# Performance work log

Hardware: AMD Instinct MI355X
Metric: run time of the kernel (lower is better)

The kernel has to match this reference:

```python
import jax, jax.numpy as jnp
import numpy as np

N_QUBITS = 8
N_LAYERS = 2


def _apply_1q(state, U, wire):
    # state: (B, 2, ..., 2) with N_QUBITS qubit axes; U: (2,2) complex, shared over batch
    s = jnp.moveaxis(state, 1 + wire, 1)
    shp = s.shape
    out = jnp.einsum('ij,bjr->bir', U, s.reshape(shp[0], 2, -1)).reshape(shp)
    return jnp.moveaxis(out, 1, 1 + wire)


def _apply_cnot(state, c, t):
    s = jnp.moveaxis(state, (1 + c, 1 + t), (1, 2))  # (B, ctrl, tgt, ...)
    s_new = jnp.stack([s[:, 0], jnp.flip(s[:, 1], axis=1)], axis=1)
    return jnp.moveaxis(s_new, (1, 2), (1 + c, 1 + t))


def _circuit(angles, q_weights):
    # angles: (B, N) real; q_weights: (L, N, 3) real
    B = angles.shape[0]
    N = N_QUBITS
    # AngleEmbedding with RY on |0...0> -> product state [cos(a/2), sin(a/2)] per qubit
    half = angles * 0.5
    state = jnp.ones((B, 1), dtype=jnp.complex64)
    for i in range(N):
        v = jnp.stack([jnp.cos(half[:, i]), jnp.sin(half[:, i])], axis=-1).astype(jnp.complex64)
        state = (state[:, :, None] * v[:, None, :]).reshape(B, -1)
    state = state.reshape((B,) + (2,) * N)
    # StronglyEntanglingLayers: per layer, Rot(phi,theta,omega) on each wire then CNOT ring
    L = q_weights.shape[0]
    for l in range(L):
        for i in range(N):
            phi = q_weights[l, i, 0]
            theta = q_weights[l, i, 1]
            omega = q_weights[l, i, 2]
            c = jnp.cos(theta * 0.5).astype(jnp.complex64)
            s_ = jnp.sin(theta * 0.5).astype(jnp.complex64)
            ep = jnp.exp(-0.5j * (phi + omega).astype(jnp.complex64))
            em = jnp.exp(-0.5j * (phi - omega).astype(jnp.complex64))
            # Rot = RZ(omega) RY(theta) RZ(phi)
            U = jnp.stack([jnp.stack([ep * c, -jnp.conj(em) * s_]),
                           jnp.stack([em * s_, jnp.conj(ep) * c])])
            state = _apply_1q(state, U, i)
        r = l % (N - 1) + 1  # default range pattern of StronglyEntanglingLayers
        for i in range(N):
            state = _apply_cnot(state, i, (i + r) % N)
    # <Z_i> = P(bit_i=0) - P(bit_i=1)
    probs = jnp.real(state * jnp.conj(state))
    zs = []
    for i in range(N):
        pm = jnp.moveaxis(probs, 1 + i, 1).reshape(B, 2, -1).sum(-1)
        zs.append(pm[:, 0] - pm[:, 1])
    return jnp.stack(zs, axis=-1)  # (B, N) real


def setup_inputs() -> dict:
    key = jax.random.key(0)
    k1, k2, k3, k4 = jax.random.split(key, 4)
    B = 32768
    pca_x = jax.random.normal(k1, (B, N_QUBITS), dtype=jnp.float32)
    q_weights = jax.random.uniform(k2, (N_LAYERS, N_QUBITS, 3), dtype=jnp.float32) * (2.0 * np.pi)
    W = jax.random.normal(k3, (N_QUBITS, 64), dtype=jnp.float32) * 0.35
    b = jax.random.normal(k4, (64,), dtype=jnp.float32) * 0.02
    gamma = jnp.ones((64,), dtype=jnp.float32)
    beta = jnp.zeros((64,), dtype=jnp.float32)
    return {"pca_x": pca_x, "q_weights": q_weights, "W": W, "b": b, "gamma": gamma, "beta": beta}


def reference(pca_x, q_weights, W, b, gamma, beta):
    angles = jax.nn.sigmoid(pca_x) * jnp.pi  # (B, 8)
    z = _circuit(angles, q_weights).astype(pca_x.dtype)  # (B, 8) PauliZ expvals
    h = z @ W + b  # (B, 64)
    mu = jnp.mean(h, axis=-1, keepdims=True)
    var = jnp.mean((h - mu) ** 2, axis=-1, keepdims=True)
    hn = (h - mu) / jnp.sqrt(var + 1e-5) * gamma + beta
    return jax.nn.gelu(hn, approximate=False)
```

## Files before the change

kernel.cpp:

```cpp
#include <hip/hip_runtime.h>
#include <math.h>

#define DEVFN __device__ __forceinline__

typedef __attribute__((ext_vector_type(8))) _Float16 f16x8;
typedef __attribute__((ext_vector_type(4))) float f32x4;

DEVFN float shxor(float v, int m) { return __shfl_xor(v, m, 64); }

template<int W>
DEVFN void rot_gate(int lane, float (&sr)[4], float (&si)[4], const float* u) {
  const float u00r=u[0], u00i=u[1], u01r=u[2], u01i=u[3];
  const float u10r=u[4], u10i=u[5], u11r=u[6], u11i=u[7];
  if constexpr (W <= 5) {
    constexpr int M = 1 << (5 - W);
    const bool hi = (lane & M) != 0;
    const float cmr = hi ? u11r : u00r, cmi = hi ? u11i : u00i;
    const float cor = hi ? u10r : u01r, coi = hi ? u10i : u01i;
    #pragma unroll
    for (int k = 0; k < 4; ++k) {
      float orr = shxor(sr[k], M);
      float oii = shxor(si[k], M);
      float nr = cmr*sr[k] - cmi*si[k] + cor*orr - coi*oii;
      float ni = cmr*si[k] + cmi*sr[k] + cor*oii + coi*orr;
      sr[k] = nr; si[k] = ni;
    }
  } else {
    constexpr int KB = (W == 6) ? 2 : 1;
    #pragma unroll
    for (int k0 = 0; k0 < 4; ++k0) {
      if ((k0 & KB) == 0) {
        const int k1 = k0 | KB;
        float ar = sr[k0], ai = si[k0];
        float br = sr[k1], bi = si[k1];
        sr[k0] = u00r*ar - u00i*ai + u01r*br - u01i*bi;
        si[k0] = u00r*ai + u00i*ar + u01r*bi + u01i*br;
        sr[k1] = u10r*ar - u10i*ai + u11r*br - u11i*bi;
        si[k1] = u10r*ai + u10i*ar + u11r*bi + u11i*br;
      }
    }
  }
}

template<int C, int T>
DEVFN void cnot_gate(int lane, float (&sr)[4], float (&si)[4]) {
  constexpr int PC = 7 - C, PT = 7 - T;
  if constexpr (PT >= 2) {
    constexpr int M = 1 << (PT - 2);
    #pragma unroll
    for (int k = 0; k < 4; ++k) {
      float orr = shxor(sr[k], M);
      float oii = shxor(si[k], M);
      bool ctrl;
      if constexpr (PC >= 2) ctrl = ((lane >> (PC - 2)) & 1) != 0;
      else                   ctrl = ((k >> PC) & 1) != 0;
      if (ctrl) { sr[k] = orr; si[k] = oii; }
    }
  } else {
    float tr[4], ti[4];
    #pragma unroll
    for (int k = 0; k < 4; ++k) { tr[k] = sr[k]; ti[k] = si[k]; }
    #pragma unroll
    for (int k = 0; k < 4; ++k) {
      bool ctrl;
      if constexpr (PC >= 2) ctrl = ((lane >> (PC - 2)) & 1) != 0;
      else                   ctrl = ((k >> PC) & 1) != 0;
      if (ctrl) { sr[k] = tr[k ^ (1 << PT)]; si[k] = ti[k ^ (1 << PT)]; }
    }
  }
}

__global__ __launch_bounds__(64) void qsb_prep(
    const float* __restrict__ qw, const float* __restrict__ Wm,
    const float* __restrict__ bias,
    _Float16* __restrict__ Bfrag, float* __restrict__ stats) {
  __shared__ float uL[16 * 8];
  int bid = blockIdx.x;
  int lane = threadIdx.x;
  if (bid < 256) {
    if (lane < 16) {
      int l = lane >> 3, i = lane & 7;
      float phi = qw[l*24 + i*3 + 0];
      float th  = qw[l*24 + i*3 + 1];
      float om  = qw[l*24 + i*3 + 2];
      float cth = cosf(0.5f*th), sth = sinf(0.5f*th);
      float ap = 0.5f*(phi+om), am = 0.5f*(phi-om);
      float cap = cosf(ap), sap = sinf(ap);
      float cam = cosf(am), sam = sinf(am);
      float* u = &uL[lane*8];
      u[0] =  cap*cth; u[1] = -sap*cth;
      u[2] = -cam*sth; u[3] = -sam*sth;
      u[4] =  cam*sth; u[5] = -sam*sth;
      u[6] =  cap*cth; u[7] =  sap*cth;
    }
    __syncthreads();
    int col = bid;
    float sr[4], si[4];
    #pragma unroll
    for (int k = 0; k < 4; ++k) { sr[k] = (lane*4 + k == col) ? 1.f : 0.f; si[k] = 0.f; }
    rot_gate<0>(lane, sr, si, &uL[0*8]);
    rot_gate<1>(lane, sr, si, &uL[1*8]);
    rot_gate<2>(lane, sr, si, &uL[2*8]);
    rot_gate<3>(lane, sr, si, &uL[3*8]);
    rot_gate<4>(lane, sr, si, &uL[4*8]);
    rot_gate<5>(lane, sr, si, &uL[5*8]);
    rot_gate<6>(lane, sr, si, &uL[6*8]);
    rot_gate<7>(lane, sr, si, &uL[7*8]);
    cnot_gate<0,1>(lane, sr, si);
    cnot_gate<1,2>(lane, sr, si);
    cnot_gate<2,3>(lane, sr, si);
    cnot_gate<3,4>(lane, sr, si);
    cnot_gate<4,5>(lane, sr, si);
    cnot_gate<5,6>(lane, sr, si);
    cnot_gate<6,7>(lane, sr, si);
    cnot_gate<7,0>(lane, sr, si);
    rot_gate<0>(lane, sr, si, &uL[(8+0)*8]);
    rot_gate<1>(lane, sr, si, &uL[(8+1)*8]);
    rot_gate<2>(lane, sr, si, &uL[(8+2)*8]);
    rot_gate<3>(lane, sr, si, &uL[(8+3)*8]);
    rot_gate<4>(lane, sr, si, &uL[(8+4)*8]);
    rot_gate<5>(lane, sr, si, &uL[(8+5)*8]);
    rot_gate<6>(lane, sr, si, &uL[(8+6)*8]);
    rot_gate<7>(lane, sr, si, &uL[(8+7)*8]);
    cnot_gate<0,2>(lane, sr, si);
    cnot_gate<1,3>(lane, sr, si);
    cnot_gate<2,4>(lane, sr, si);
    cnot_gate<3,5>(lane, sr, si);
    cnot_gate<4,6>(lane, sr, si);
    cnot_gate<5,7>(lane, sr, si);
    cnot_gate<6,0>(lane, sr, si);
    cnot_gate<7,1>(lane, sr, si);
    const int ks = col >> 5, kg = (col >> 3) & 3, e = col & 7;
    #pragma unroll
    for (int k = 0; k < 4; ++k) {
      int a = lane*4 + k;
      int ch = a >> 5, nf = (a >> 4) & 1, cf = a & 15;
      int pos = (kg*16 + cf)*8 + e;
      Bfrag[((ch*4 + nf    )*8 + ks)*512 + pos] = (_Float16)sr[k];
      Bfrag[((ch*4 + 2 + nf)*8 + ks)*512 + pos] = (_Float16)si[k];
    }
  } else {
    int t = lane;
    {
      int i = t >> 3, j = t & 7;
      float s = 0.f;
      for (int c = 0; c < 64; ++c) s += Wm[i*64 + c] * Wm[j*64 + c];
      stats[16 + t] = s * 0.015625f;
    }
    if (t < 8) {
      float s = 0.f, sb = 0.f;
      for (int c = 0; c < 64; ++c) { float w = Wm[t*64 + c]; s += w; sb += w * bias[c]; }
      stats[t]     = s * 0.015625f;
      stats[8 + t] = 2.f * sb * 0.015625f;
    }
    if (t == 0) {
      float s = 0.f, s2 = 0.f;
      for (int c = 0; c < 64; ++c) { s += bias[c]; s2 += bias[c]*bias[c]; }
      stats[80] = s * 0.015625f;
      stats[81] = s2 * 0.015625f;
    }
  }
}

__global__ __launch_bounds__(256, 4) void qsb_main(
    const float* __restrict__ pca, const _Float16* __restrict__ Bfrag,
    const float* __restrict__ statsG,
    const float* __restrict__ Wm, const float* __restrict__ bias,
    const float* __restrict__ gamma, const float* __restrict__ beta,
    float* __restrict__ out, int B) {
  __shared__ __align__(16) _Float16 A3[8192];
  __shared__ __align__(16) _Float16 YL[4 * 1280];
  __shared__ float zpart[2304];
  __shared__ float zrow[256];
  __shared__ float musig[64];
  __shared__ float Wl[512];
  __shared__ float biasL[64], gammaL[64], betaL[64];
  __shared__ float statsL[82];

  const int tid = threadIdx.x;
  const int wid = tid >> 6, lane = tid & 63;
  const int cfrag = lane & 15, kgrp = lane >> 4;
  const int r0 = blockIdx.x * 32;

  #pragma unroll
  for (int i = tid; i < 512; i += 256) Wl[i] = Wm[i];
  if (tid >= 256 - 64) {
    int t = tid - (256 - 64);
    biasL[t] = bias[t]; gammaL[t] = gamma[t]; betaL[t] = beta[t];
  }
  if (tid < 82) statsL[tid] = statsG[tid];

  f16x8 sfrag;
  #pragma unroll
  for (int e = 0; e < 8; ++e) {
    float v;
    if      (cfrag == 0) v = 1.f;
    else if (cfrag == 1) v = (kgrp & 2) ? -1.f : 1.f;
    else if (cfrag == 2) v = (kgrp & 1) ? -1.f : 1.f;
    else if (cfrag == 3) v = (e & 4)    ? -1.f : 1.f;
    else if (cfrag == 4) v = (e & 2)    ? -1.f : 1.f;
    else if (cfrag == 5) v = (e & 1)    ? -1.f : 1.f;
    else v = 0.f;
    sfrag[e] = (_Float16)v;
  }

  {
    const int rl = tid >> 3, tq = tid & 7;
    const int r = r0 + rl;
    float cv[8], sv[8];
    #pragma unroll
    for (int w = 0; w < 8; ++w) { cv[w] = 1.f; sv[w] = 0.f; }
    if (r < B) {
      #pragma unroll
      for (int w = 0; w < 8; ++w) {
        float x = pca[r*8 + w];
        float sg = __builtin_amdgcn_rcpf(1.f + __expf(-x));
        float ang = 1.5707963267948966f * sg;
        cv[w] = __cosf(ang); sv[w] = __sinf(ang);
      }
    }
    float base = ((tq & 4) ? sv[0] : cv[0]) * ((tq & 2) ? sv[1] : cv[1])
               * ((tq & 1) ? sv[2] : cv[2]);
    float arr[32];
    arr[0] = base;
    #pragma unroll
    for (int p = 0; p < 5; ++p) {
      const int w = 7 - p;
      const int sz = 1 << p;
      #pragma unroll
      for (int i = 0; i < (1 << p); ++i) {
        arr[i + sz] = arr[i] * sv[w];
        arr[i]      = arr[i] * cv[w];
      }
    }
    _Float16* dstBase = &A3[((tq*2 + (rl >> 4))*16 + (rl & 15))*32];
    #pragma unroll
    for (int ib = 0; ib < 4; ++ib) {
      f16x8 v;
      #pragma unroll
      for (int j = 0; j < 8; ++j) v[j] = (_Float16)arr[ib*8 + j];
      *(f16x8*)(dstBase + (ib ^ (tq & 3))*8) = v;
    }
  }
  __syncthreads();

  _Float16* Yw = &YL[wid * 1280];
  const _Float16* BwBase = Bfrag + (size_t)(wid*2) * 16384 + lane*8;

  f32x4 acc[2][4];
  #pragma unroll
  for (int m = 0; m < 2; ++m)
    #pragma unroll
    for (int q = 0; q < 4; ++q) acc[m][q] = (f32x4){0.f, 0.f, 0.f, 0.f};

  f16x8 bk[3][4];
  #pragma unroll
  for (int q = 0; q < 4; ++q) bk[0][q] = *(const f16x8*)(BwBase + 0*512 + q*4096);
  #pragma unroll
  for (int q = 0; q < 4; ++q) bk[1][q] = *(const f16x8*)(BwBase + 1*512 + q*4096);

  #pragma unroll
  for (int s = 0; s < 16; ++s) {
    const int ks = s & 7;
    const int bi = s % 3;
    if (s + 2 < 16) {
      const int bj = (s + 2) % 3;
      const int c2 = (s + 2) >> 3, ks2 = (s + 2) & 7;
      const _Float16* p2 = BwBase + c2*16384 + ks2*512;
      #pragma unroll
      for (int q = 0; q < 4; ++q) bk[bj][q] = *(const f16x8*)(p2 + q*4096);
    }
    {
      f16x8 af0 = *(const f16x8*)&A3[((ks*2 + 0)*16 + cfrag)*32 + (kgrp ^ (ks & 3))*8];
      f16x8 af1 = *(const f16x8*)&A3[((ks*2 + 1)*16 + cfrag)*32 + (kgrp ^ (ks & 3))*8];
      #pragma unroll
      for (int q = 0; q < 4; ++q) {
        acc[0][q] = __builtin_amdgcn_mfma_f32_16x16x32_f16(af0, bk[bi][q], acc[0][q], 0, 0, 0);
        acc[1][q] = __builtin_amdgcn_mfma_f32_16x16x32_f16(af1, bk[bi][q], acc[1][q], 0, 0, 0);
      }
    }
    if (ks == 7) {
      const int ch = wid*2 + (s >> 3);
      #pragma unroll
      for (int m = 0; m < 2; ++m) {
        #pragma unroll
        for (int nf = 0; nf < 2; ++nf) {
          #pragma unroll
          for (int j = 0; j < 4; ++j) {
            float re = acc[m][nf][j], im = acc[m][2 + nf][j];
            float p = re*re + im*im;
            Yw[m*640 + (kgrp*4 + j)*40 + nf*16 + cfrag] = (_Float16)p;
          }
        }
      }
      #pragma unroll
      for (int m = 0; m < 2; ++m) {
        f16x8 yfrag = *(const f16x8*)&Yw[m*640 + (lane & 15)*40 + kgrp*8];
        f32x4 d = __builtin_amdgcn_mfma_f32_16x16x32_f16(yfrag, sfrag, (f32x4){0.f,0.f,0.f,0.f}, 0, 0, 0);
        if (cfrag < 6) {
          #pragma unroll
          for (int j = 0; j < 4; ++j)
            zpart[(ch*32 + m*16 + kgrp*4 + j)*9 + cfrag] = d[j];
        }
      }
      #pragma unroll
      for (int m = 0; m < 2; ++m)
        #pragma unroll
        for (int q = 0; q < 4; ++q) acc[m][q] = (f32x4){0.f, 0.f, 0.f, 0.f};
    }
  }
  __syncthreads();

  {
    const int row = tid >> 3, w = tid & 7;
    const int slot = (w < 3) ? 0 : (w - 2);
    const int sm = (w == 0) ? 4 : (w == 1) ? 2 : (w == 2) ? 1 : 0;
    float z = 0.f;
    #pragma unroll
    for (int ch = 0; ch < 8; ++ch) {
      float v = zpart[(ch*32 + row)*9 + slot];
      z += (ch & sm) ? -v : v;
    }
    zrow[row*8 + w] = z;
    f32x4 zlo = *(const f32x4*)&zrow[row*8];
    f32x4 zhi = *(const f32x4*)&zrow[row*8 + 4];
    float zj[8] = {zlo[0], zlo[1], zlo[2], zlo[3], zhi[0], zhi[1], zhi[2], zhi[3]};
    float qi = statsL[8 + w];
    #pragma unroll
    for (int j = 0; j < 8; ++j) qi += statsL[16 + w*8 + j] * zj[j];
    float e2p = zj[w] * qi;
    float mup = statsL[w] * zj[w];
    e2p += shxor(e2p, 1); e2p += shxor(e2p, 2); e2p += shxor(e2p, 4);
    mup += shxor(mup, 1); mup += shxor(mup, 2); mup += shxor(mup, 4);
    if (w == 0) {
      float mu = mup + statsL[80];
      float e2 = e2p + statsL[81];
      float var = e2 - mu*mu;
      musig[row*2]     = mu;
      musig[row*2 + 1] = rsqrtf(fmaxf(var, 0.f) + 1e-5f);
    }
  }

  #pragma unroll
  for (int rr = 0; rr < 8; ++rr) {
    const int row = wid*8 + rr;
    const int gr = r0 + row;
    float h = biasL[lane];
    #pragma unroll
    for (int i = 0; i < 8; ++i) h = fmaf(zrow[row*8 + i], Wl[i*64 + lane], h);
    float hn = (h - musig[row*2]) * musig[row*2 + 1] * gammaL[lane] + betaL[lane];
    float ge = 0.5f * hn * (1.f + erff(hn * 0.70710678118654752f));
    if (gr < B) out[gr*64 + lane] = ge;
  }
}

extern "C" void kernel_launch(void* const* d_in, const int* in_sizes, int n_in,
                              void* d_out, int out_size, void* d_ws, size_t ws_size,
                              hipStream_t stream) {
  const float* pca   = (const float*)d_in[0];
  const float* qw    = (const float*)d_in[1];
  const float* Wm    = (const float*)d_in[2];
  const float* bias  = (const float*)d_in[3];
  const float* gamma = (const float*)d_in[4];
  const float* beta  = (const float*)d_in[5];
  float* out = (float*)d_out;

  _Float16* Bfrag = (_Float16*)d_ws;
  float* stats = (float*)((char*)d_ws + 512*256*2);

  int B = in_sizes[0] / 8;

  hipLaunchKernelGGL(qsb_prep, dim3(257), dim3(64), 0, stream, qw, Wm, bias, Bfrag, stats);
  int blocks = (B + 31) / 32;
  hipLaunchKernelGGL(qsb_main, dim3(blocks), dim3(256), 0, stream,
                     pca, Bfrag, stats, Wm, bias, gamma, beta, out, B);
}
```

Baseline: 28.58 us.

## Double rows per block so each B fragment feeds four MFMA row tiles

Result: slower. 29.27 us (+2.4%).

```diff
diff --git a/kernel.cpp b/kernel.cpp
--- a/kernel.cpp
+++ b/kernel.cpp
@@ -162,17 +162,17 @@
   }
 }
 
-__global__ __launch_bounds__(256, 4) void qsb_main(
+__global__ __launch_bounds__(256, 2) void qsb_main(
     const float* __restrict__ pca, const _Float16* __restrict__ Bfrag,
     const float* __restrict__ statsG,
     const float* __restrict__ Wm, const float* __restrict__ bias,
     const float* __restrict__ gamma, const float* __restrict__ beta,
     float* __restrict__ out, int B) {
-  __shared__ __align__(16) _Float16 A3[8192];
-  __shared__ __align__(16) _Float16 YL[4 * 1280];
-  __shared__ float zpart[2304];
-  __shared__ float zrow[256];
-  __shared__ float musig[64];
+  __shared__ __align__(16) _Float16 A3[16384];
+  __shared__ __align__(16) _Float16 YL[4 * 2560];
+  __shared__ float zpart[4608];
+  __shared__ float zrow[512];
+  __shared__ float musig[128];
   __shared__ float Wl[512];
   __shared__ float biasL[64], gammaL[64], betaL[64];
   __shared__ float statsL[82];
@@ -180,7 +180,7 @@
   const int tid = threadIdx.x;
   const int wid = tid >> 6, lane = tid & 63;
   const int cfrag = lane & 15, kgrp = lane >> 4;
-  const int r0 = blockIdx.x * 32;
+  const int r0 = blockIdx.x * 64;
 
   #pragma unroll
   for (int i = tid; i < 512; i += 256) Wl[i] = Wm[i];
@@ -205,7 +205,7 @@
   }
 
   {
-    const int rl = tid >> 3, tq = tid & 7;
+    const int rl = tid >> 2, tq = tid & 3;
     const int r = r0 + rl;
     float cv[8], sv[8];
     #pragma unroll
@@ -219,12 +219,11 @@
         cv[w] = __cosf(ang); sv[w] = __sinf(ang);
       }
     }
-    float base = ((tq & 4) ? sv[0] : cv[0]) * ((tq & 2) ? sv[1] : cv[1])
-               * ((tq & 1) ? sv[2] : cv[2]);
-    float arr[32];
+    float base = ((tq & 2) ? sv[0] : cv[0]) * ((tq & 1) ? sv[1] : cv[1]);
+    float arr[64];
     arr[0] = base;
     #pragma unroll
-    for (int p = 0; p < 5; ++p) {
+    for (int p = 0; p < 6; ++p) {
       const int w = 7 - p;
       const int sz = 1 << p;
       #pragma unroll
@@ -233,23 +232,27 @@
         arr[i]      = arr[i] * cv[w];
       }
     }
-    _Float16* dstBase = &A3[((tq*2 + (rl >> 4))*16 + (rl & 15))*32];
-    #pragma unroll
-    for (int ib = 0; ib < 4; ++ib) {
+    const int m = rl >> 4, cf = rl & 15;
+    const int cfx = (cf >> 1) & 3;
+    #pragma unroll
+    for (int ib = 0; ib < 8; ++ib) {
+      const int ks = tq*2 + (ib >> 2);
+      const int slot = (ib & 3) ^ (ks & 3) ^ cfx;
       f16x8 v;
       #pragma unroll
       for (int j = 0; j < 8; ++j) v[j] = (_Float16)arr[ib*8 + j];
-      *(f16x8*)(dstBase + (ib ^ (tq & 3))*8) = v;
+      *(f16x8*)&A3[((ks*4 + m)*16 + cf)*32 + slot*8] = v;
     }
   }
   __syncthreads();
 
-  _Float16* Yw = &YL[wid * 1280];
+  _Float16* Yw = &YL[wid * 2560];
   const _Float16* BwBase = Bfrag + (size_t)(wid*2) * 16384 + lane*8;
-
-  f32x4 acc[2][4];
-  #pragma unroll
-  for (int m = 0; m < 2; ++m)
+  const int cfx = (cfrag >> 1) & 3;
+
+  f32x4 acc[4][4];
+  #pragma unroll
+  for (int m = 0; m < 4; ++m)
     #pragma unroll
     for (int q = 0; q < 4; ++q) acc[m][q] = (f32x4){0.f, 0.f, 0.f, 0.f};
 
@@ -271,18 +274,22 @@
       for (int q = 0; q < 4; ++q) bk[bj][q] = *(const f16x8*)(p2 + q*4096);
     }
     {
-      f16x8 af0 = *(const f16x8*)&A3[((ks*2 + 0)*16 + cfrag)*32 + (kgrp ^ (ks & 3))*8];
-      f16x8 af1 = *(const f16x8*)&A3[((ks*2 + 1)*16 + cfrag)*32 + (kgrp ^ (ks & 3))*8];
+      const int slot = (kgrp ^ (ks & 3) ^ cfx)*8;
+      f16x8 af[4];
+      #pragma unroll
+      for (int m = 0; m < 4; ++m)
+        af[m] = *(const f16x8*)&A3[((ks*4 + m)*16 + cfrag)*32 + slot];
       #pragma unroll
       for (int q = 0; q < 4; ++q) {
-        acc[0][q] = __builtin_amdgcn_mfma_f32_16x16x32_f16(af0, bk[bi][q], acc[0][q], 0, 0, 0);
-        acc[1][q] = __builtin_amdgcn_mfma_f32_16x16x32_f16(af1, bk[bi][q], acc[1][q], 0, 0, 0);
+        #pragma unroll
+        for (int m = 0; m < 4; ++m)
+          acc[m][q] = __builtin_amdgcn_mfma_f32_16x16x32_f16(af[m], bk[bi][q], acc[m][q], 0, 0, 0);
       }
     }
     if (ks == 7) {
       const int ch = wid*2 + (s >> 3);
       #pragma unroll
-      for (int m = 0; m < 2; ++m) {
+      for (int m = 0; m < 4; ++m) {
         #pragma unroll
         for (int nf = 0; nf < 2; ++nf) {
           #pragma unroll
@@ -294,31 +301,32 @@
         }
       }
       #pragma unroll
-      for (int m = 0; m < 2; ++m) {
+      for (int m = 0; m < 4; ++m) {
         f16x8 yfrag = *(const f16x8*)&Yw[m*640 + (lane & 15)*40 + kgrp*8];
         f32x4 d = __builtin_amdgcn_mfma_f32_16x16x32_f16(yfrag, sfrag, (f32x4){0.f,0.f,0.f,0.f}, 0, 0, 0);
         if (cfrag < 6) {
           #pragma unroll
           for (int j = 0; j < 4; ++j)
-            zpart[(ch*32 + m*16 + kgrp*4 + j)*9 + cfrag] = d[j];
+            zpart[(ch*64 + m*16 + kgrp*4 + j)*9 + cfrag] = d[j];
         }
       }
       #pragma unroll
-      for (int m = 0; m < 2; ++m)
+      for (int m = 0; m < 4; ++m)
         #pragma unroll
         for (int q = 0; q < 4; ++q) acc[m][q] = (f32x4){0.f, 0.f, 0.f, 0.f};
     }
   }
   __syncthreads();
 
-  {
-    const int row = tid >> 3, w = tid & 7;
+  #pragma unroll
+  for (int h = 0; h < 2; ++h) {
+    const int row = h*32 + (tid >> 3), w = tid & 7;
     const int slot = (w < 3) ? 0 : (w - 2);
     const int sm = (w == 0) ? 4 : (w == 1) ? 2 : (w == 2) ? 1 : 0;
     float z = 0.f;
     #pragma unroll
     for (int ch = 0; ch < 8; ++ch) {
-      float v = zpart[(ch*32 + row)*9 + slot];
+      float v = zpart[(ch*64 + row)*9 + slot];
       z += (ch & sm) ? -v : v;
     }
     zrow[row*8 + w] = z;
@@ -342,15 +350,18 @@
   }
 
   #pragma unroll
-  for (int rr = 0; rr < 8; ++rr) {
-    const int row = wid*8 + rr;
-    const int gr = r0 + row;
-    float h = biasL[lane];
-    #pragma unroll
-    for (int i = 0; i < 8; ++i) h = fmaf(zrow[row*8 + i], Wl[i*64 + lane], h);
-    float hn = (h - musig[row*2]) * musig[row*2 + 1] * gammaL[lane] + betaL[lane];
-    float ge = 0.5f * hn * (1.f + erff(hn * 0.70710678118654752f));
-    if (gr < B) out[gr*64 + lane] = ge;
+  for (int h = 0; h < 2; ++h) {
+    #pragma unroll
+    for (int rr = 0; rr < 8; ++rr) {
+      const int row = h*32 + wid*8 + rr;
+      const int gr = r0 + row;
+      float hv = biasL[lane];
+      #pragma unroll
+      for (int i = 0; i < 8; ++i) hv = fmaf(zrow[row*8 + i], Wl[i*64 + lane], hv);
+      float hn = (hv - musig[row*2]) * musig[row*2 + 1] * gammaL[lane] + betaL[lane];
+      float ge = 0.5f * hn * (1.f + erff(hn * 0.70710678118654752f));
+      if (gr < B) out[gr*64 + lane] = ge;
+    }
   }
 }
 
@@ -371,7 +382,7 @@
   int B = in_sizes[0] / 8;
 
   hipLaunchKernelGGL(qsb_prep, dim3(257), dim3(64), 0, stream, qw, Wm, bias, Bfrag, stats);
-  int blocks = (B + 31) / 32;
+  int blocks = (B + 63) / 64;
   hipLaunchKernelGGL(qsb_main, dim3(blocks), dim3(256), 0, stream,
                      pca, Bfrag, stats, Wm, bias, gamma, beta, out, B);
 }
```

## Give each wave 16 whole rows across all chunks, building A fragments in registers

Applied to the files above, without the earlier changes.

New measurement: 50.60 us. +77.0%, slower.

```diff
diff --git a/kernel.cpp b/kernel.cpp
--- a/kernel.cpp
+++ b/kernel.cpp
@@ -168,11 +168,9 @@
     const float* __restrict__ Wm, const float* __restrict__ bias,
     const float* __restrict__ gamma, const float* __restrict__ beta,
     float* __restrict__ out, int B) {
-  __shared__ __align__(16) _Float16 A3[8192];
-  __shared__ __align__(16) _Float16 YL[4 * 1280];
-  __shared__ float zpart[2304];
-  __shared__ float zrow[256];
-  __shared__ float musig[64];
+  __shared__ __align__(16) _Float16 YL[4 * 640];
+  __shared__ __align__(16) float zrowL[4 * 192];
+  __shared__ float musigL[4 * 32];
   __shared__ float Wl[512];
   __shared__ float biasL[64], gammaL[64], betaL[64];
   __shared__ float statsL[82];
@@ -180,7 +178,7 @@
   const int tid = threadIdx.x;
   const int wid = tid >> 6, lane = tid & 63;
   const int cfrag = lane & 15, kgrp = lane >> 4;
-  const int r0 = blockIdx.x * 32;
+  const int r0w = blockIdx.x * 64 + wid * 16;
 
   #pragma unroll
   for (int i = tid; i < 512; i += 256) Wl[i] = Wm[i];
@@ -189,141 +187,121 @@
     biasL[t] = bias[t]; gammaL[t] = gamma[t]; betaL[t] = beta[t];
   }
   if (tid < 82) statsL[tid] = statsG[tid];
-
-  f16x8 sfrag;
-  #pragma unroll
-  for (int e = 0; e < 8; ++e) {
-    float v;
-    if      (cfrag == 0) v = 1.f;
-    else if (cfrag == 1) v = (kgrp & 2) ? -1.f : 1.f;
-    else if (cfrag == 2) v = (kgrp & 1) ? -1.f : 1.f;
-    else if (cfrag == 3) v = (e & 4)    ? -1.f : 1.f;
-    else if (cfrag == 4) v = (e & 2)    ? -1.f : 1.f;
-    else if (cfrag == 5) v = (e & 1)    ? -1.f : 1.f;
-    else v = 0.f;
-    sfrag[e] = (_Float16)v;
-  }
-
+  __syncthreads();
+
+  _Float16* Yw = &YL[wid * 640];
+  float* zrowW = &zrowL[wid * 192];
+  float* musigW = &musigL[wid * 32];
+
+  f16x8 af[8];
   {
-    const int rl = tid >> 3, tq = tid & 7;
-    const int r = r0 + rl;
-    float cv[8], sv[8];
-    #pragma unroll
-    for (int w = 0; w < 8; ++w) { cv[w] = 1.f; sv[w] = 0.f; }
+    const int r = r0w + cfrag;
+    float c[8], s[8];
+    #pragma unroll
+    for (int w = 0; w < 8; ++w) { c[w] = 1.f; s[w] = 0.f; }
     if (r < B) {
       #pragma unroll
       for (int w = 0; w < 8; ++w) {
         float x = pca[r*8 + w];
         float sg = __builtin_amdgcn_rcpf(1.f + __expf(-x));
         float ang = 1.5707963267948966f * sg;
-        cv[w] = __cosf(ang); sv[w] = __sinf(ang);
-      }
-    }
-    float base = ((tq & 4) ? sv[0] : cv[0]) * ((tq & 2) ? sv[1] : cv[1])
-               * ((tq & 1) ? sv[2] : cv[2]);
-    float arr[32];
-    arr[0] = base;
-    #pragma unroll
-    for (int p = 0; p < 5; ++p) {
+        c[w] = __cosf(ang); s[w] = __sinf(ang);
+      }
+    }
+    float tail[8];
+    tail[0] = 1.f;
+    #pragma unroll
+    for (int p = 0; p < 3; ++p) {
       const int w = 7 - p;
       const int sz = 1 << p;
       #pragma unroll
       for (int i = 0; i < (1 << p); ++i) {
-        arr[i + sz] = arr[i] * sv[w];
-        arr[i]      = arr[i] * cv[w];
-      }
-    }
-    _Float16* dstBase = &A3[((tq*2 + (rl >> 4))*16 + (rl & 15))*32];
-    #pragma unroll
-    for (int ib = 0; ib < 4; ++ib) {
-      f16x8 v;
-      #pragma unroll
-      for (int j = 0; j < 8; ++j) v[j] = (_Float16)arr[ib*8 + j];
-      *(f16x8*)(dstBase + (ib ^ (tq & 3))*8) = v;
-    }
-  }
-  __syncthreads();
-
-  _Float16* Yw = &YL[wid * 1280];
-  const _Float16* BwBase = Bfrag + (size_t)(wid*2) * 16384 + lane*8;
-
-  f32x4 acc[2][4];
+        tail[i + sz] = tail[i] * s[w];
+        tail[i]      = tail[i] * c[w];
+      }
+    }
+    float pre[8];
+    pre[0] = ((kgrp & 2) ? s[3] : c[3]) * ((kgrp & 1) ? s[4] : c[4]);
+    #pragma unroll
+    for (int p = 0; p < 3; ++p) {
+      const int w = 2 - p;
+      const int sz = 1 << p;
+      #pragma unroll
+      for (int i = 0; i < (1 << p); ++i) {
+        pre[i + sz] = pre[i] * s[w];
+        pre[i]      = pre[i] * c[w];
+      }
+    }
+    #pragma unroll
+    for (int ks = 0; ks < 8; ++ks) {
+      #pragma unroll
+      for (int e = 0; e < 8; ++e)
+        af[ks][e] = (_Float16)(pre[ks] * tail[e]);
+    }
+  }
+
+  f32x4 zacc = (f32x4){0.f, 0.f, 0.f, 0.f};
   #pragma unroll
-  for (int m = 0; m < 2; ++m)
-    #pragma unroll
-    for (int q = 0; q < 4; ++q) acc[m][q] = (f32x4){0.f, 0.f, 0.f, 0.f};
-
-  f16x8 bk[3][4];
+  for (int ch = 0; ch < 8; ++ch) {
+    const _Float16* Bw = Bfrag + (size_t)ch * 16384 + lane*8;
+
+    f32x4 acc[4];
+    #pragma unroll
+    for (int q = 0; q < 4; ++q) acc[q] = (f32x4){0.f, 0.f, 0.f, 0.f};
+
+    #pragma unroll
+    for (int ks = 0; ks < 8; ++ks) {
+      f16x8 bq0 = *(const f16x8*)(Bw + (0*8 + ks)*512);
+      f16x8 bq1 = *(const f16x8*)(Bw + (1*8 + ks)*512);
+      f16x8 bq2 = *(const f16x8*)(Bw + (2*8 + ks)*512);
+      f16x8 bq3 = *(const f16x8*)(Bw + (3*8 + ks)*512);
+      acc[0] = __builtin_amdgcn_mfma_f32_16x16x32_f16(af[ks], bq0, acc[0], 0, 0, 0);
+      acc[1] = __builtin_amdgcn_mfma_f32_16x16x32_f16(af[ks], bq1, acc[1], 0, 0, 0);
+      acc[2] = __builtin_amdgcn_mfma_f32_16x16x32_f16(af[ks], bq2, acc[2], 0, 0, 0);
+      acc[3] = __builtin_amdgcn_mfma_f32_16x16x32_f16(af[ks], bq3, acc[3], 0, 0, 0);
+    }
+
+    #pragma unroll
+    for (int nf = 0; nf < 2; ++nf) {
+      #pragma unroll
+      for (int j = 0; j < 4; ++j) {
+        float re = acc[nf][j], im = acc[2 + nf][j];
+        float p = re*re + im*im;
+        Yw[(kgrp*4 + j)*40 + nf*16 + cfrag] = (_Float16)p;
+      }
+    }
+
+    f16x8 sfc;
+    #pragma unroll
+    for (int e = 0; e < 8; ++e) {
+      float v;
+      if      (cfrag == 0) v = (ch & 4) ? -1.f : 1.f;
+      else if (cfrag == 1) v = (ch & 2) ? -1.f : 1.f;
+      else if (cfrag == 2) v = (ch & 1) ? -1.f : 1.f;
+      else if (cfrag == 3) v = (kgrp & 2) ? -1.f : 1.f;
+      else if (cfrag == 4) v = (kgrp & 1) ? -1.f : 1.f;
+      else if (cfrag == 5) v = (e & 4) ? -1.f : 1.f;
+      else if (cfrag == 6) v = (e & 2) ? -1.f : 1.f;
+      else if (cfrag == 7) v = (e & 1) ? -1.f : 1.f;
+      else v = 0.f;
+      sfc[e] = (_Float16)v;
+    }
+
+    f16x8 yfrag = *(const f16x8*)&Yw[(lane & 15)*40 + kgrp*8];
+    zacc = __builtin_amdgcn_mfma_f32_16x16x32_f16(yfrag, sfc, zacc, 0, 0, 0);
+  }
+
+  if (cfrag < 8) {
+    #pragma unroll
+    for (int j = 0; j < 4; ++j)
+      zrowW[(kgrp*4 + j)*12 + cfrag] = zacc[j];
+  }
+
   #pragma unroll
-  for (int q = 0; q < 4; ++q) bk[0][q] = *(const f16x8*)(BwBase + 0*512 + q*4096);
-  #pragma unroll
-  for (int q = 0; q < 4; ++q) bk[1][q] = *(const f16x8*)(BwBase + 1*512 + q*4096);
-
-  #pragma unroll
-  for (int s = 0; s < 16; ++s) {
-    const int ks = s & 7;
-    const int bi = s % 3;
-    if (s + 2 < 16) {
-      const int bj = (s + 2) % 3;
-      const int c2 = (s + 2) >> 3, ks2 = (s + 2) & 7;
-      const _Float16* p2 = BwBase + c2*16384 + ks2*512;
-      #pragma unroll
-      for (int q = 0; q < 4; ++q) bk[bj][q] = *(const f16x8*)(p2 + q*4096);
-    }
-    {
-      f16x8 af0 = *(const f16x8*)&A3[((ks*2 + 0)*16 + cfrag)*32 + (kgrp ^ (ks & 3))*8];
-      f16x8 af1 = *(const f16x8*)&A3[((ks*2 + 1)*16 + cfrag)*32 + (kgrp ^ (ks & 3))*8];
-      #pragma unroll
-      for (int q = 0; q < 4; ++q) {
-        acc[0][q] = __builtin_amdgcn_mfma_f32_16x16x32_f16(af0, bk[bi][q], acc[0][q], 0, 0, 0);
-        acc[1][q] = __builtin_amdgcn_mfma_f32_16x16x32_f16(af1, bk[bi][q], acc[1][q], 0, 0, 0);
-      }
-    }
-    if (ks == 7) {
-      const int ch = wid*2 + (s >> 3);
-      #pragma unroll
-      for (int m = 0; m < 2; ++m) {
-        #pragma unroll
-        for (int nf = 0; nf < 2; ++nf) {
-          #pragma unroll
-          for (int j = 0; j < 4; ++j) {
-            float re = acc[m][nf][j], im = acc[m][2 + nf][j];
-            float p = re*re + im*im;
-            Yw[m*640 + (kgrp*4 + j)*40 + nf*16 + cfrag] = (_Float16)p;
-          }
-        }
-      }
-      #pragma unroll
-      for (int m = 0; m < 2; ++m) {
-        f16x8 yfrag = *(const f16x8*)&Yw[m*640 + (lane & 15)*40 + kgrp*8];
-        f32x4 d = __builtin_amdgcn_mfma_f32_16x16x32_f16(yfrag, sfrag, (f32x4){0.f,0.f,0.f,0.f}, 0, 0, 0);
-        if (cfrag < 6) {
-          #pragma unroll
-          for (int j = 0; j < 4; ++j)
-            zpart[(ch*32 + m*16 + kgrp*4 + j)*9 + cfrag] = d[j];
-        }
-      }
-      #pragma unroll
-      for (int m = 0; m < 2; ++m)
-        #pragma unroll
-        for (int q = 0; q < 4; ++q) acc[m][q] = (f32x4){0.f, 0.f, 0.f, 0.f};
-    }
-  }
-  __syncthreads();
-
-  {
-    const int row = tid >> 3, w = tid & 7;
-    const int slot = (w < 3) ? 0 : (w - 2);
-    const int sm = (w == 0) ? 4 : (w == 1) ? 2 : (w == 2) ? 1 : 0;
-    float z = 0.f;
-    #pragma unroll
-    for (int ch = 0; ch < 8; ++ch) {
-      float v = zpart[(ch*32 + row)*9 + slot];
-      z += (ch & sm) ? -v : v;
-    }
-    zrow[row*8 + w] = z;
-    f32x4 zlo = *(const f32x4*)&zrow[row*8];
-    f32x4 zhi = *(const f32x4*)&zrow[row*8 + 4];
+  for (int pass = 0; pass < 2; ++pass) {
+    const int row = pass*8 + (lane >> 3), w = lane & 7;
+    f32x4 zlo = *(const f32x4*)&zrowW[row*12];
+    f32x4 zhi = *(const f32x4*)&zrowW[row*12 + 4];
     float zj[8] = {zlo[0], zlo[1], zlo[2], zlo[3], zhi[0], zhi[1], zhi[2], zhi[3]};
     float qi = statsL[8 + w];
     #pragma unroll
@@ -336,21 +314,30 @@
       float mu = mup + statsL[80];
       float e2 = e2p + statsL[81];
       float var = e2 - mu*mu;
-      musig[row*2]     = mu;
-      musig[row*2 + 1] = rsqrtf(fmaxf(var, 0.f) + 1e-5f);
-    }
-  }
-
-  #pragma unroll
-  for (int rr = 0; rr < 8; ++rr) {
-    const int row = wid*8 + rr;
-    const int gr = r0 + row;
-    float h = biasL[lane];
-    #pragma unroll
-    for (int i = 0; i < 8; ++i) h = fmaf(zrow[row*8 + i], Wl[i*64 + lane], h);
-    float hn = (h - musig[row*2]) * musig[row*2 + 1] * gammaL[lane] + betaL[lane];
-    float ge = 0.5f * hn * (1.f + erff(hn * 0.70710678118654752f));
-    if (gr < B) out[gr*64 + lane] = ge;
+      musigW[row*2]     = mu;
+      musigW[row*2 + 1] = rsqrtf(fmaxf(var, 0.f) + 1e-5f);
+    }
+  }
+
+  {
+    float wcol[8];
+    #pragma unroll
+    for (int i = 0; i < 8; ++i) wcol[i] = Wl[i*64 + lane];
+    const float bl = biasL[lane], gl = gammaL[lane], btl = betaL[lane];
+    #pragma unroll
+    for (int row = 0; row < 16; ++row) {
+      f32x4 zlo = *(const f32x4*)&zrowW[row*12];
+      f32x4 zhi = *(const f32x4*)&zrowW[row*12 + 4];
+      float h = bl;
+      h = fmaf(zlo[0], wcol[0], h); h = fmaf(zlo[1], wcol[1], h);
+      h = fmaf(zlo[2], wcol[2], h); h = fmaf(zlo[3], wcol[3], h);
+      h = fmaf(zhi[0], wcol[4], h); h = fmaf(zhi[1], wcol[5], h);
+      h = fmaf(zhi[2], wcol[6], h); h = fmaf(zhi[3], wcol[7], h);
+      float hn = (h - musigW[row*2]) * musigW[row*2 + 1] * gl + btl;
+      float ge = 0.5f * hn * (1.f + erff(hn * 0.70710678118654752f));
+      const int gr = r0w + row;
+      if (gr < B) out[gr*64 + lane] = ge;
+    }
   }
 }
 
@@ -371,7 +358,7 @@
   int B = in_sizes[0] / 8;
 
   hipLaunchKernelGGL(qsb_prep, dim3(257), dim3(64), 0, stream, qw, Wm, bias, Bfrag, stats);
-  int blocks = (B + 31) / 32;
+  int blocks = (B + 63) / 64;
   hipLaunchKernelGGL(qsb_main, dim3(blocks), dim3(256), 0, stream,
                      pca, Bfrag, stats, Wm, bias, gamma, beta, out, B);
 }
```
